# Kernel tuning notes

Measured on AMD Instinct MI355X. Metric: run time of the kernel, lower is better.

Reference implementation:

```python
import jax, jax.numpy as jnp
import numpy as np

BS, N, HEADS, DIN, DOUT = 512, 128, 8, 64, 64


def setup_inputs() -> dict:
    key = jax.random.key(0)
    k1, k2, k3, k4, k5 = jax.random.split(key, 5)
    h = jax.random.normal(k1, (BS, N, DIN), dtype=jnp.float32)
    w = jax.random.normal(k2, (HEADS, DIN, DOUT), dtype=jnp.float32) * 0.1
    a_src = jax.random.normal(k3, (HEADS, DOUT, 1), dtype=jnp.float32) * 0.1
    a_dst = jax.random.normal(k4, (HEADS, DOUT, 1), dtype=jnp.float32) * 0.1
    bias = jnp.zeros((DOUT,), dtype=jnp.float32)
    # sparse random adjacency with self-loops so every softmax row is valid
    adj = jax.random.uniform(k5, (BS, N, N)) < 0.05
    adj = adj | jnp.eye(N, dtype=bool)[None, :, :]
    return {"h": h, "adj": adj, "w": w, "a_src": a_src, "a_dst": a_dst, "bias": bias}


def reference(h, adj, w, a_src, a_dst, bias):
    # h: [b, n, i]; w: [H, i, o] -> h_prime: [b, H, n, o]
    h_prime = jnp.einsum('bni,hio->bhno', h, w)
    t = jnp.tanh(h_prime)
    attn_src = jnp.einsum('bhno,ho->bhn', t, a_src[..., 0])  # [b, H, n]
    attn_dst = jnp.einsum('bhno,ho->bhn', t, a_dst[..., 0])  # [b, H, n]
    # attn[b,h,i,j] = src[b,h,i] + dst[b,h,j]
    attn = attn_src[..., :, None] + attn_dst[..., None, :]
    attn = jax.nn.leaky_relu(attn, negative_slope=0.2)
    attn = jnp.where(adj[:, None, :, :], attn, -jnp.inf)
    attn = jax.nn.softmax(attn, axis=-1)
    out = jnp.einsum('bhij,bhjo->bhio', attn, h_prime)
    return out + bias
```

## Files before the change

### kernel.cpp

```cpp
#include <hip/hip_runtime.h>

#define BSZ 512
#define NN 128
#define HEADS 8
#define DIN 64
#define DOUT 64

typedef __bf16 bf16x8 __attribute__((ext_vector_type(8)));
typedef float floatx4 __attribute__((ext_vector_type(4)));

static __device__ __forceinline__ unsigned short f2bf(float f) {
    __bf16 b = (__bf16)f;
    return __builtin_bit_cast(unsigned short, b);
}
static __device__ __forceinline__ bf16x8 ld_frag(const unsigned short* p) {
    uint4 r = *reinterpret_cast<const uint4*>(p);
    return __builtin_bit_cast(bf16x8, r);
}

__global__ __launch_bounds__(512, 4) void gat_fwd(
    const float* __restrict__ hin,
    const int*   __restrict__ adj,
    const float* __restrict__ w,
    const float* __restrict__ a_src,
    const float* __restrict__ a_dst,
    const float* __restrict__ bias,
    float* __restrict__ out)
{
    __shared__ __attribute__((aligned(16))) unsigned short h_lds[NN * DIN];
    __shared__ __attribute__((aligned(16))) unsigned short wT[DOUT * DIN];
    __shared__ __attribute__((aligned(16))) unsigned short hpT[DOUT * NN];
    __shared__ __attribute__((aligned(16))) unsigned int   msk[NN * 4];
    __shared__ __attribute__((aligned(16))) float s_src[NN];
    __shared__ __attribute__((aligned(16))) float s_dst[NN];

    const int b    = blockIdx.x;
    const int tid  = threadIdx.x;
    const int lane = tid & 63;
    const int wv   = tid >> 6;
    const int lg   = lane >> 4;
    const int lm   = lane & 15;

    const float* hb = hin + (size_t)b * NN * DIN;
    #pragma unroll
    for (int q = 0; q < 4; ++q) {
        const int flat = q * 2048 + tid * 4;
        const int n = flat >> 6, k = flat & 63;
        float4 v = *reinterpret_cast<const float4*>(hb + flat);
        unsigned int lo = f2bf(v.x) | ((unsigned int)f2bf(v.y) << 16);
        unsigned int hi = f2bf(v.z) | ((unsigned int)f2bf(v.w) << 16);
        const int idx = (n * 64 + k) ^ ((n & 7) << 3);
        *reinterpret_cast<uint2*>(&h_lds[idx]) = make_uint2(lo, hi);
    }
    const int* adjb = adj + (size_t)b * NN * NN;
    for (int it = 0; it < 32; ++it) {
        const int idx = wv * 2048 + it * 64 + lane;
        unsigned long long m = __ballot(adjb[idx] != 0);
        if (lane == 0) {
            const int row = idx >> 7, half = (idx >> 6) & 1;
            msk[row * 4 + half * 2]     = (unsigned int)m;
            msk[row * 4 + half * 2 + 1] = (unsigned int)(m >> 32);
        }
    }
    auto stage_w = [&](int hd) {
        const float* wg = w + hd * DIN * DOUT;
        const int o = tid & 63, kb = (tid >> 6) * 8;
        unsigned int u[4];
        #pragma unroll
        for (int p = 0; p < 4; ++p) {
            float f0 = wg[(kb + 2 * p) * DOUT + o];
            float f1 = wg[(kb + 2 * p + 1) * DOUT + o];
            u[p] = f2bf(f0) | ((unsigned int)f2bf(f1) << 16);
        }
        const int idx = (o * 64 + kb) ^ ((o & 7) << 3);
        *reinterpret_cast<uint4*>(&wT[idx]) = make_uint4(u[0], u[1], u[2], u[3]);
    };
    stage_w(0);
    __syncthreads();

    float* outb = out + (size_t)b * HEADS * NN * DOUT;
    const int n0 = wv * 16;

    for (int hd = 0; hd < HEADS; ++hd) {
        floatx4 acc[4] = {floatx4{0,0,0,0}, floatx4{0,0,0,0}, floatx4{0,0,0,0}, floatx4{0,0,0,0}};
        #pragma unroll
        for (int kt = 0; kt < 2; ++kt) {
            const int an = n0 + lm;
            bf16x8 af = ld_frag(&h_lds[(an * 64 + kt * 32 + lg * 8) ^ ((an & 7) << 3)]);
            #pragma unroll
            for (int nt = 0; nt < 4; ++nt) {
                const int o = nt * 16 + lm;
                bf16x8 bfr = ld_frag(&wT[(o * 64 + kt * 32 + lg * 8) ^ ((o & 7) << 3)]);
                acc[nt] = __builtin_amdgcn_mfma_f32_16x16x32_bf16(af, bfr, acc[nt], 0, 0, 0);
            }
        }
        const float* asp = a_src + hd * DOUT;
        const float* adp = a_dst + hd * DOUT;
        float ps[4] = {0, 0, 0, 0}, pd[4] = {0, 0, 0, 0};
        #pragma unroll
        for (int nt = 0; nt < 4; ++nt) {
            const int o = nt * 16 + lm;
            const float as = asp[o], ad = adp[o];
            #pragma unroll
            for (int r = 0; r < 4; ++r) {
                const float v = acc[nt][r];
                const float ex = __expf(2.f * v);
                const float t = 1.f - 2.f / (ex + 1.f);
                ps[r] = fmaf(t, as, ps[r]);
                pd[r] = fmaf(t, ad, pd[r]);
            }
            const int jb = n0 + lg * 4;
            unsigned int u01 = f2bf(acc[nt][0]) | ((unsigned int)f2bf(acc[nt][1]) << 16);
            unsigned int u23 = f2bf(acc[nt][2]) | ((unsigned int)f2bf(acc[nt][3]) << 16);
            const int base = (o * 128 + jb) ^ ((o & 7) << 3);
            *reinterpret_cast<unsigned int*>(&hpT[base])     = u01;
            *reinterpret_cast<unsigned int*>(&hpT[base + 2]) = u23;
        }
        #pragma unroll
        for (int r = 0; r < 4; ++r) {
            #pragma unroll
            for (int m = 1; m <= 8; m <<= 1) {
                ps[r] += __shfl_xor(ps[r], m);
                pd[r] += __shfl_xor(pd[r], m);
            }
        }
        if (lm == 0) {
            #pragma unroll
            for (int r = 0; r < 4; ++r) {
                s_src[n0 + lg * 4 + r] = ps[r];
                s_dst[n0 + lg * 4 + r] = pd[r];
            }
        }
        __syncthreads();

        if (hd + 1 < HEADS) stage_w(hd + 1);

        const int i = n0 + lm;
        uint4 mr = *reinterpret_cast<const uint4*>(&msk[i * 4]);
        const unsigned int mw[4] = {mr.x, mr.y, mr.z, mr.w};
        const float si = s_src[i];

        float mx = -3.0e38f;
        #pragma unroll
        for (int kt = 0; kt < 4; ++kt) {
            float4 d0 = *reinterpret_cast<const float4*>(&s_dst[kt * 32 + lg * 8]);
            float4 d1 = *reinterpret_cast<const float4*>(&s_dst[kt * 32 + lg * 8 + 4]);
            const float dv[8] = {d0.x, d0.y, d0.z, d0.w, d1.x, d1.y, d1.z, d1.w};
            #pragma unroll
            for (int q = 0; q < 8; ++q) {
                const bool bit = (mw[kt] >> (lg * 8 + q)) & 1;
                mx = fmaxf(mx, bit ? (si + dv[q]) : -3.0e38f);
            }
        }
        mx = fmaxf(mx, __shfl_xor(mx, 16));
        mx = fmaxf(mx, __shfl_xor(mx, 32));
        const float mxl = fmaxf(mx, 0.f) + 0.2f * fminf(mx, 0.f);

        float sum = 0.f;
        bf16x8 af2[4];
        #pragma unroll
        for (int kt = 0; kt < 4; ++kt) {
            float4 d0 = *reinterpret_cast<const float4*>(&s_dst[kt * 32 + lg * 8]);
            float4 d1 = *reinterpret_cast<const float4*>(&s_dst[kt * 32 + lg * 8 + 4]);
            const float dv[8] = {d0.x, d0.y, d0.z, d0.w, d1.x, d1.y, d1.z, d1.w};
            bf16x8 a;
            #pragma unroll
            for (int q = 0; q < 8; ++q) {
                const float x = si + dv[q];
                const float xl = fmaxf(x, 0.f) + 0.2f * fminf(x, 0.f);
                const bool bit = (mw[kt] >> (lg * 8 + q)) & 1;
                const float e = __expf((bit ? xl : -3.0e38f) - mxl);
                sum += e;
                a[q] = (__bf16)e;
            }
            af2[kt] = a;
        }
        sum += __shfl_xor(sum, 16);
        sum += __shfl_xor(sum, 32);
        const float inv = 1.f / sum;

        floatx4 oacc[4] = {floatx4{0,0,0,0}, floatx4{0,0,0,0}, floatx4{0,0,0,0}, floatx4{0,0,0,0}};
        #pragma unroll
        for (int kt = 0; kt < 4; ++kt) {
            #pragma unroll
            for (int nt = 0; nt < 4; ++nt) {
                const int o = nt * 16 + lm;
                bf16x8 bfr = ld_frag(&hpT[(o * 128 + kt * 32 + lg * 8) ^ ((o & 7) << 3)]);
                oacc[nt] = __builtin_amdgcn_mfma_f32_16x16x32_bf16(af2[kt], bfr, oacc[nt], 0, 0, 0);
            }
        }
        float invr[4];
        #pragma unroll
        for (int r = 0; r < 4; ++r) invr[r] = __shfl(inv, lg * 4 + r);
        #pragma unroll
        for (int nt = 0; nt < 4; ++nt) {
            const int o = nt * 16 + lm;
            const float bo = bias[o];
            #pragma unroll
            for (int r = 0; r < 4; ++r) {
                const int row = n0 + lg * 4 + r;
                outb[(size_t)hd * NN * DOUT + row * DOUT + o] = fmaf(oacc[nt][r], invr[r], bo);
            }
        }
        __syncthreads();
    }
}

extern "C" void kernel_launch(void* const* d_in, const int* in_sizes, int n_in,
                              void* d_out, int out_size, void* d_ws, size_t ws_size,
                              hipStream_t stream) {
    (void)in_sizes; (void)n_in; (void)out_size; (void)d_ws; (void)ws_size;
    const float* h     = (const float*)d_in[0];
    const int*   adj   = (const int*)d_in[1];
    const float* w     = (const float*)d_in[2];
    const float* a_src = (const float*)d_in[3];
    const float* a_dst = (const float*)d_in[4];
    const float* bias  = (const float*)d_in[5];
    float* out = (float*)d_out;
    gat_fwd<<<dim3(BSZ), dim3(512), 0, stream>>>(h, adj, w, a_src, a_dst, bias, out);
}
```

Baseline: 76.22 us.

## Sparse softmax via mask-bit iteration into LDS P, keep h fragments in registers

The masked softmax now visits only the set adjacency bits of each row, using ctz iteration. It writes bf16 exp values into a zeroed, swizzled LDS P matrix that feeds the attention MFMA, instead of computing exp for all 128 columns. The separate row-max pass is dropped, which relies on the logits being bounded by tanh and the attention weights. The h tile is converted straight into per-wave register MFMA fragments rather than staged through LDS, and bias loads are hoisted out of the head loop. LDS footprint grows with the 32KB P buffer, which may lower occupancy, and the per-lane bit loop adds some divergence.

```diff
diff --git a/kernel.cpp b/kernel.cpp
--- a/kernel.cpp
+++ b/kernel.cpp
@@ -27,9 +27,9 @@
     const float* __restrict__ bias,
     float* __restrict__ out)
 {
-    __shared__ __attribute__((aligned(16))) unsigned short h_lds[NN * DIN];
     __shared__ __attribute__((aligned(16))) unsigned short wT[DOUT * DIN];
     __shared__ __attribute__((aligned(16))) unsigned short hpT[DOUT * NN];
+    __shared__ __attribute__((aligned(16))) unsigned short P[NN * NN];
     __shared__ __attribute__((aligned(16))) unsigned int   msk[NN * 4];
     __shared__ __attribute__((aligned(16))) float s_src[NN];
     __shared__ __attribute__((aligned(16))) float s_dst[NN];
@@ -40,18 +40,21 @@
     const int wv   = tid >> 6;
     const int lg   = lane >> 4;
     const int lm   = lane & 15;
+    const int n0   = wv * 16;
 
     const float* hb = hin + (size_t)b * NN * DIN;
+    bf16x8 hA[2];
     #pragma unroll
-    for (int q = 0; q < 4; ++q) {
-        const int flat = q * 2048 + tid * 4;
-        const int n = flat >> 6, k = flat & 63;
-        float4 v = *reinterpret_cast<const float4*>(hb + flat);
-        unsigned int lo = f2bf(v.x) | ((unsigned int)f2bf(v.y) << 16);
-        unsigned int hi = f2bf(v.z) | ((unsigned int)f2bf(v.w) << 16);
-        const int idx = (n * 64 + k) ^ ((n & 7) << 3);
-        *reinterpret_cast<uint2*>(&h_lds[idx]) = make_uint2(lo, hi);
+    for (int kt = 0; kt < 2; ++kt) {
+        const float* p = hb + (n0 + lm) * DIN + kt * 32 + lg * 8;
+        float4 v0 = *reinterpret_cast<const float4*>(p);
+        float4 v1 = *reinterpret_cast<const float4*>(p + 4);
+        bf16x8 a;
+        a[0] = (__bf16)v0.x; a[1] = (__bf16)v0.y; a[2] = (__bf16)v0.z; a[3] = (__bf16)v0.w;
+        a[4] = (__bf16)v1.x; a[5] = (__bf16)v1.y; a[6] = (__bf16)v1.z; a[7] = (__bf16)v1.w;
+        hA[kt] = a;
     }
+
     const int* adjb = adj + (size_t)b * NN * NN;
     for (int it = 0; it < 32; ++it) {
         const int idx = wv * 2048 + it * 64 + lane;
@@ -79,19 +82,19 @@
     __syncthreads();
 
     float* outb = out + (size_t)b * HEADS * NN * DOUT;
-    const int n0 = wv * 16;
+    float bo[4];
+    #pragma unroll
+    for (int nt = 0; nt < 4; ++nt) bo[nt] = bias[nt * 16 + lm];
 
     for (int hd = 0; hd < HEADS; ++hd) {
         floatx4 acc[4] = {floatx4{0,0,0,0}, floatx4{0,0,0,0}, floatx4{0,0,0,0}, floatx4{0,0,0,0}};
         #pragma unroll
         for (int kt = 0; kt < 2; ++kt) {
-            const int an = n0 + lm;
-            bf16x8 af = ld_frag(&h_lds[(an * 64 + kt * 32 + lg * 8) ^ ((an & 7) << 3)]);
             #pragma unroll
             for (int nt = 0; nt < 4; ++nt) {
                 const int o = nt * 16 + lm;
                 bf16x8 bfr = ld_frag(&wT[(o * 64 + kt * 32 + lg * 8) ^ ((o & 7) << 3)]);
-                acc[nt] = __builtin_amdgcn_mfma_f32_16x16x32_bf16(af, bfr, acc[nt], 0, 0, 0);
+                acc[nt] = __builtin_amdgcn_mfma_f32_16x16x32_bf16(hA[kt], bfr, acc[nt], 0, 0, 0);
             }
         }
         const float* asp = a_src + hd * DOUT;
@@ -136,44 +139,24 @@
         if (hd + 1 < HEADS) stage_w(hd + 1);
 
         const int i = n0 + lm;
-        uint4 mr = *reinterpret_cast<const uint4*>(&msk[i * 4]);
-        const unsigned int mw[4] = {mr.x, mr.y, mr.z, mr.w};
+        const int sw = (i & 7) << 3;
         const float si = s_src[i];
 
-        float mx = -3.0e38f;
-        #pragma unroll
-        for (int kt = 0; kt < 4; ++kt) {
-            float4 d0 = *reinterpret_cast<const float4*>(&s_dst[kt * 32 + lg * 8]);
-            float4 d1 = *reinterpret_cast<const float4*>(&s_dst[kt * 32 + lg * 8 + 4]);
-            const float dv[8] = {d0.x, d0.y, d0.z, d0.w, d1.x, d1.y, d1.z, d1.w};
-            #pragma unroll
-            for (int q = 0; q < 8; ++q) {
-                const bool bit = (mw[kt] >> (lg * 8 + q)) & 1;
-                mx = fmaxf(mx, bit ? (si + dv[q]) : -3.0e38f);
-            }
-        }
-        mx = fmaxf(mx, __shfl_xor(mx, 16));
-        mx = fmaxf(mx, __shfl_xor(mx, 32));
-        const float mxl = fmaxf(mx, 0.f) + 0.2f * fminf(mx, 0.f);
-
+        const int pz = i * 128 + lg * 32;
+        #pragma unroll
+        for (int t = 0; t < 4; ++t)
+            *reinterpret_cast<uint4*>(&P[(pz + 8 * t) ^ sw]) = make_uint4(0, 0, 0, 0);
+
+        unsigned int m = msk[i * 4 + lg];
         float sum = 0.f;
-        bf16x8 af2[4];
-        #pragma unroll
-        for (int kt = 0; kt < 4; ++kt) {
-            float4 d0 = *reinterpret_cast<const float4*>(&s_dst[kt * 32 + lg * 8]);
-            float4 d1 = *reinterpret_cast<const float4*>(&s_dst[kt * 32 + lg * 8 + 4]);
-            const float dv[8] = {d0.x, d0.y, d0.z, d0.w, d1.x, d1.y, d1.z, d1.w};
-            bf16x8 a;
-            #pragma unroll
-            for (int q = 0; q < 8; ++q) {
-                const float x = si + dv[q];
-                const float xl = fmaxf(x, 0.f) + 0.2f * fminf(x, 0.f);
-                const bool bit = (mw[kt] >> (lg * 8 + q)) & 1;
-                const float e = __expf((bit ? xl : -3.0e38f) - mxl);
-                sum += e;
-                a[q] = (__bf16)e;
-            }
-            af2[kt] = a;
+        while (m) {
+            const int q = __builtin_ctz(m); m &= m - 1;
+            const float x = si + s_dst[lg * 32 + q];
+            const float xl = fmaxf(x, 0.f) + 0.2f * fminf(x, 0.f);
+            const float e = __expf(xl);
+            const __bf16 eb = (__bf16)e;
+            sum += (float)eb;
+            P[(pz + q) ^ sw] = __builtin_bit_cast(unsigned short, eb);
         }
         sum += __shfl_xor(sum, 16);
         sum += __shfl_xor(sum, 32);
@@ -182,11 +165,12 @@
         floatx4 oacc[4] = {floatx4{0,0,0,0}, floatx4{0,0,0,0}, floatx4{0,0,0,0}, floatx4{0,0,0,0}};
         #pragma unroll
         for (int kt = 0; kt < 4; ++kt) {
+            const bf16x8 af = ld_frag(&P[(i * 128 + kt * 32 + lg * 8) ^ sw]);
             #pragma unroll
             for (int nt = 0; nt < 4; ++nt) {
                 const int o = nt * 16 + lm;
                 bf16x8 bfr = ld_frag(&hpT[(o * 128 + kt * 32 + lg * 8) ^ ((o & 7) << 3)]);
-                oacc[nt] = __builtin_amdgcn_mfma_f32_16x16x32_bf16(af2[kt], bfr, oacc[nt], 0, 0, 0);
+                oacc[nt] = __builtin_amdgcn_mfma_f32_16x16x32_bf16(af, bfr, oacc[nt], 0, 0, 0);
             }
         }
         float invr[4];
@@ -195,11 +179,10 @@
         #pragma unroll
         for (int nt = 0; nt < 4; ++nt) {
             const int o = nt * 16 + lm;
-            const float bo = bias[o];
             #pragma unroll
             for (int r = 0; r < 4; ++r) {
                 const int row = n0 + lg * 4 + r;
-                outb[(size_t)hd * NN * DOUT + row * DOUT + o] = fmaf(oacc[nt][r], invr[r], bo);
+                outb[(size_t)hd * NN * DOUT + row * DOUT + o] = fmaf(oacc[nt][r], invr[r], bo[nt]);
             }
         }
         __syncthreads();
```

New measurement: 66.94 us. -12.2%, faster.
